# Kernel tuning notes

Measured on AMD Instinct MI355X. Metric: run time of the kernel, lower is better.

The kernel has to match this reference:

```python
import jax, jax.numpy as jnp
import numpy as np

V, D, H, C = 100000, 300, 16, 5
B, T = 256, 128


def setup_inputs() -> dict:
    key = jax.random.key(0)
    ks = jax.random.split(key, 8)
    s = 1.0 / np.sqrt(H).astype(np.float32)  # PyTorch LSTM/Linear init range
    x = jax.random.randint(ks[0], (B, T), 0, V)
    emb = jax.random.normal(ks[1], (V, D), jnp.float32) * 0.02
    W_ih = jax.random.uniform(ks[2], (4 * H, D), jnp.float32, -s, s)
    W_hh = jax.random.uniform(ks[3], (4 * H, H), jnp.float32, -s, s)
    b_ih = jax.random.uniform(ks[4], (4 * H,), jnp.float32, -s, s)
    b_hh = jax.random.uniform(ks[5], (4 * H,), jnp.float32, -s, s)
    W_out = jax.random.uniform(ks[6], (C, H), jnp.float32, -s, s)
    b_out = jax.random.uniform(ks[7], (C,), jnp.float32, -s, s)
    return dict(x=x, emb=emb, W_ih=W_ih, W_hh=W_hh, b_ih=b_ih, b_hh=b_hh,
                W_out=W_out, b_out=b_out)


def reference(x, emb, W_ih, W_hh, b_ih, b_hh, W_out, b_out):
    h_dim = W_hh.shape[1]
    xe = emb[x]  # [B,T,D] embedding lookup
    # Precompute input contribution to all 4 gates for all timesteps (one big GEMM).
    xg = jnp.einsum('btd,gd->btg', xe, W_ih) + b_ih + b_hh  # [B,T,4H]
    xg = jnp.transpose(xg, (1, 0, 2))  # [T,B,4H] time-major for scan
    b = x.shape[0]
    h0 = jnp.zeros((b, h_dim), xg.dtype)
    c0 = jnp.zeros((b, h_dim), xg.dtype)

    def step(carry, g_t):
        h, c = carry
        g = g_t + h @ W_hh.T  # [B,4H]
        i, f, gg, o = jnp.split(g, 4, axis=-1)  # PyTorch gate order: i,f,g,o
        i = jax.nn.sigmoid(i)
        f = jax.nn.sigmoid(f)
        gg = jnp.tanh(gg)
        o = jax.nn.sigmoid(o)
        c = f * c + i * gg
        h = o * jnp.tanh(c)
        return (h, c), h

    _, hs = jax.lax.scan(step, (h0, c0), xg)  # hs: [T,B,H]
    hs = jnp.transpose(hs, (1, 0, 2))  # [B,T,H]
    return hs @ W_out.T + b_out  # [B,T,C]
```

## Files before the change

### kernel.cpp

```cpp
#include <hip/hip_runtime.h>
#include <cstdint>

#define BB 256
#define TT 128
#define DD 300
#define HH 16
#define GG 64
#define CC 5
#define KC 60
#define NCH 5

__global__ __launch_bounds__(256) void lstm_fused_kernel(
    const int* __restrict__ x, const float* __restrict__ emb,
    const float* __restrict__ W_ih, const float* __restrict__ W_hh,
    const float* __restrict__ b_ih, const float* __restrict__ b_hh,
    const float* __restrict__ W_out, const float* __restrict__ b_out,
    float* __restrict__ out) {

  __shared__ float As[TT * KC];
  __shared__ float Ws[KC * 68];
  __shared__ float xgs[TT * GG];
  __shared__ float hsm[TT * HH];
  __shared__ int   xid[TT];

  const int t  = threadIdx.x;
  const int b  = blockIdx.x;
  const int tx = t & 15;
  const int ty = t >> 4;

  if (t < TT) xid[t] = x[b * TT + t];
  __syncthreads();

  const int na = (t < 128) ? 8 : 7;
  const int nw = (t < 192) ? 4 : 3;

  float4 apf[8];
  float4 wpf[4];

  auto load_chunk = [&](int dbase) {
#pragma unroll
    for (int i = 0; i < 8; i++) {
      if (i < na) {
        int u = t + 256 * i;
        int r = u / 15, f = u - r * 15;
        apf[i] = *(const float4*)(emb + (size_t)xid[r] * DD + dbase + 4 * f);
      }
    }
#pragma unroll
    for (int i = 0; i < 4; i++) {
      if (i < nw) {
        int u = t + 256 * i;
        int c = u / 15, f = u - c * 15;
        wpf[i] = *(const float4*)(W_ih + c * DD + dbase + 4 * f);
      }
    }
  };

  auto store_chunk = [&]() {
#pragma unroll
    for (int i = 0; i < 8; i++) {
      if (i < na) {
        int u = t + 256 * i;
        int r = u / 15, f = u - r * 15;
        *(float4*)&As[r * KC + 4 * f] = apf[i];
      }
    }
#pragma unroll
    for (int i = 0; i < 4; i++) {
      if (i < nw) {
        int u = t + 256 * i;
        int c = u / 15, f = u - c * 15;
        Ws[(4 * f + 0) * 68 + c] = wpf[i].x;
        Ws[(4 * f + 1) * 68 + c] = wpf[i].y;
        Ws[(4 * f + 2) * 68 + c] = wpf[i].z;
        Ws[(4 * f + 3) * 68 + c] = wpf[i].w;
      }
    }
  };

  float acc[8][4] = {};

  load_chunk(0);
  for (int ch = 0; ch < NCH; ch++) {
    if (ch > 0) __syncthreads();
    store_chunk();
    __syncthreads();
    if (ch + 1 < NCH) load_chunk((ch + 1) * KC);

#pragma unroll
    for (int q = 0; q < 15; q++) {
      float4 wc[4];
#pragma unroll
      for (int j = 0; j < 4; j++)
        wc[j] = *(const float4*)&Ws[(q * 4 + j) * 68 + tx * 4];
#pragma unroll
      for (int r = 0; r < 8; r++) {
        const int row = ty + 16 * r;
        float4 a = *(const float4*)&As[row * KC + q * 4];
#pragma unroll
        for (int c = 0; c < 4; c++) {
          acc[r][c] = fmaf(a.x, ((const float*)&wc[0])[c], acc[r][c]);
          acc[r][c] = fmaf(a.y, ((const float*)&wc[1])[c], acc[r][c]);
          acc[r][c] = fmaf(a.z, ((const float*)&wc[2])[c], acc[r][c]);
          acc[r][c] = fmaf(a.w, ((const float*)&wc[3])[c], acc[r][c]);
        }
      }
    }
  }

  float bias[4];
#pragma unroll
  for (int c = 0; c < 4; c++)
    bias[c] = b_ih[tx * 4 + c] + b_hh[tx * 4 + c];
#pragma unroll
  for (int r = 0; r < 8; r++) {
    const int row = ty + 16 * r;
    float4 o;
    o.x = acc[r][0] + bias[0];
    o.y = acc[r][1] + bias[1];
    o.z = acc[r][2] + bias[2];
    o.w = acc[r][3] + bias[3];
    *(float4*)&xgs[row * GG + tx * 4] = o;
  }
  __syncthreads();

  if (t < 64) {
    const int lane = t;
    const int k = lane & 15;
    const int gate = lane >> 4;
    const bool is_tanh = (gate == 2);
    const float L2E = 1.4426950408889634f;
    const float gscale = is_tanh ? (-2.0f * L2E) : (-L2E);

    float wh[16];
    {
      const float* wr = W_hh + lane * HH;
#pragma unroll
      for (int kk = 0; kk < 16; kk++) wh[kk] = wr[kk];
    }

    float c = 0.0f;
    float hu[16];
#pragma unroll
    for (int kk = 0; kk < 16; kk++) hu[kk] = 0.0f;

    float g = xgs[lane];
    for (int tstep = 0; tstep < TT; tstep++) {
      float gnext = xgs[((tstep + 1) & 127) * GG + lane];

      float a0 = fmaf(hu[0], wh[0], g);
      a0 = fmaf(hu[1], wh[1], a0);
      a0 = fmaf(hu[2], wh[2], a0);
      a0 = fmaf(hu[3], wh[3], a0);
      float a1 = hu[4] * wh[4];
      a1 = fmaf(hu[5], wh[5], a1);
      a1 = fmaf(hu[6], wh[6], a1);
      a1 = fmaf(hu[7], wh[7], a1);
      float a2 = hu[8] * wh[8];
      a2 = fmaf(hu[9], wh[9], a2);
      a2 = fmaf(hu[10], wh[10], a2);
      a2 = fmaf(hu[11], wh[11], a2);
      float a3 = hu[12] * wh[12];
      a3 = fmaf(hu[13], wh[13], a3);
      a3 = fmaf(hu[14], wh[14], a3);
      a3 = fmaf(hu[15], wh[15], a3);
      float gv_ = (a0 + a1) + (a2 + a3);

      float e = exp2f(gv_ * gscale);
      float s = __builtin_amdgcn_rcpf(1.0f + e);
      float act = is_tanh ? (2.0f * s - 1.0f) : s;

      float iv = __shfl(act, k);
      float fv = __shfl(act, k + 16);
      float gg = __shfl(act, k + 32);
      float ov = __shfl(act, k + 48);

      c = fmaf(fv, c, iv * gg);
      float e2 = exp2f(-2.0f * L2E * c);
      float tc = fmaf(2.0f, __builtin_amdgcn_rcpf(1.0f + e2), -1.0f);
      float hnew = ov * tc;

      if (lane < 16) hsm[tstep * HH + lane] = hnew;

#pragma unroll
      for (int kk = 0; kk < 16; kk++)
        hu[kk] = __uint_as_float(__builtin_amdgcn_readlane(__float_as_uint(hnew), kk));

      g = gnext;
    }
  }
  __syncthreads();

  float* outb = out + (size_t)b * TT * CC;
  for (int idx = t; idx < TT * CC; idx += 256) {
    int tt = idx / CC;
    int cc = idx - tt * CC;
    const float* wr = W_out + cc * HH;
    float accv = b_out[cc];
#pragma unroll
    for (int kk = 0; kk < 16; kk++) accv = fmaf(hsm[tt * HH + kk], wr[kk], accv);
    outb[idx] = accv;
  }
}

extern "C" void kernel_launch(void* const* d_in, const int* in_sizes, int n_in,
                              void* d_out, int out_size, void* d_ws, size_t ws_size,
                              hipStream_t stream) {
  const int*   x     = (const int*)d_in[0];
  const float* emb   = (const float*)d_in[1];
  const float* W_ih  = (const float*)d_in[2];
  const float* W_hh  = (const float*)d_in[3];
  const float* b_ih  = (const float*)d_in[4];
  const float* b_hh  = (const float*)d_in[5];
  const float* W_out = (const float*)d_in[6];
  const float* b_out = (const float*)d_in[7];
  float* out = (float*)d_out;

  lstm_fused_kernel<<<BB, 256, 0, stream>>>(x, emb, W_ih, W_hh, b_ih, b_hh,
                                            W_out, b_out, out);
}
```

Before: 236.5 us.

## Split fused LSTM into separate input-GEMM and recurrence kernels via workspace

Replaces the single fused kernel with two launches. The first is a GEMM over 64-row tiles (512 blocks) that gathers embeddings, multiplies by W_ih with an XOR-swizzled weight tile, and writes gate preactivations to a global workspace. The second is a one-wavefront-per-batch recurrence that streams xg chunks into shared memory while the scan runs, interleaves gate lanes so gate exchange uses DPP quad permutes instead of shuffles, and computes the output projection. This spreads the GEMM over more blocks and makes the serial recurrence a lighter kernel, at the cost of a global round trip for xg and a second launch.

```diff
diff --git a/kernel.cpp b/kernel.cpp
--- a/kernel.cpp
+++ b/kernel.cpp
@@ -8,38 +8,31 @@
 #define GG 64
 #define CC 5
 #define KC 60
-#define NCH 5
-
-__global__ __launch_bounds__(256) void lstm_fused_kernel(
+
+__global__ __launch_bounds__(256) void xg_gemm_kernel(
     const int* __restrict__ x, const float* __restrict__ emb,
-    const float* __restrict__ W_ih, const float* __restrict__ W_hh,
-    const float* __restrict__ b_ih, const float* __restrict__ b_hh,
-    const float* __restrict__ W_out, const float* __restrict__ b_out,
-    float* __restrict__ out) {
-
-  __shared__ float As[TT * KC];
-  __shared__ float Ws[KC * 68];
-  __shared__ float xgs[TT * GG];
-  __shared__ float hsm[TT * HH];
-  __shared__ int   xid[TT];
+    const float* __restrict__ W_ih, const float* __restrict__ b_ih,
+    const float* __restrict__ b_hh, float* __restrict__ xg) {
+
+  __shared__ float As[64 * KC];
+  __shared__ float Ws[KC * 64];
+  __shared__ int   xid[64];
 
   const int t  = threadIdx.x;
-  const int b  = blockIdx.x;
   const int tx = t & 15;
   const int ty = t >> 4;
-
-  if (t < TT) xid[t] = x[b * TT + t];
+  const int row0 = blockIdx.x * 64;
+
+  if (t < 64) xid[t] = x[row0 + t];
   __syncthreads();
 
-  const int na = (t < 128) ? 8 : 7;
-  const int nw = (t < 192) ? 4 : 3;
-
-  float4 apf[8];
-  float4 wpf[4];
+  const int na = (t < 192) ? 4 : 3;
+
+  float4 apf[4], wpf[4];
 
   auto load_chunk = [&](int dbase) {
 #pragma unroll
-    for (int i = 0; i < 8; i++) {
+    for (int i = 0; i < 4; i++) {
       if (i < na) {
         int u = t + 256 * i;
         int r = u / 15, f = u - r * 15;
@@ -48,7 +41,7 @@
     }
 #pragma unroll
     for (int i = 0; i < 4; i++) {
-      if (i < nw) {
+      if (i < na) {
         int u = t + 256 * i;
         int c = u / 15, f = u - c * 15;
         wpf[i] = *(const float4*)(W_ih + c * DD + dbase + 4 * f);
@@ -58,7 +51,7 @@
 
   auto store_chunk = [&]() {
 #pragma unroll
-    for (int i = 0; i < 8; i++) {
+    for (int i = 0; i < 4; i++) {
       if (i < na) {
         int u = t + 256 * i;
         int r = u / 15, f = u - r * 15;
@@ -67,42 +60,43 @@
     }
 #pragma unroll
     for (int i = 0; i < 4; i++) {
-      if (i < nw) {
+      if (i < na) {
         int u = t + 256 * i;
         int c = u / 15, f = u - c * 15;
-        Ws[(4 * f + 0) * 68 + c] = wpf[i].x;
-        Ws[(4 * f + 1) * 68 + c] = wpf[i].y;
-        Ws[(4 * f + 2) * 68 + c] = wpf[i].z;
-        Ws[(4 * f + 3) * 68 + c] = wpf[i].w;
+        int cp = (((c >> 2) ^ f) << 2) | (c & 3);
+        const float* w = (const float*)&wpf[i];
+        Ws[(4 * f + 0) * 64 + cp] = w[0];
+        Ws[(4 * f + 1) * 64 + cp] = w[1];
+        Ws[(4 * f + 2) * 64 + cp] = w[2];
+        Ws[(4 * f + 3) * 64 + cp] = w[3];
       }
     }
   };
 
-  float acc[8][4] = {};
+  float acc[4][4] = {};
 
   load_chunk(0);
-  for (int ch = 0; ch < NCH; ch++) {
+  for (int ch = 0; ch < 5; ch++) {
     if (ch > 0) __syncthreads();
     store_chunk();
     __syncthreads();
-    if (ch + 1 < NCH) load_chunk((ch + 1) * KC);
+    if (ch + 1 < 5) load_chunk((ch + 1) * KC);
 
 #pragma unroll
     for (int q = 0; q < 15; q++) {
       float4 wc[4];
 #pragma unroll
       for (int j = 0; j < 4; j++)
-        wc[j] = *(const float4*)&Ws[(q * 4 + j) * 68 + tx * 4];
-#pragma unroll
-      for (int r = 0; r < 8; r++) {
-        const int row = ty + 16 * r;
-        float4 a = *(const float4*)&As[row * KC + q * 4];
-#pragma unroll
-        for (int c = 0; c < 4; c++) {
-          acc[r][c] = fmaf(a.x, ((const float*)&wc[0])[c], acc[r][c]);
-          acc[r][c] = fmaf(a.y, ((const float*)&wc[1])[c], acc[r][c]);
-          acc[r][c] = fmaf(a.z, ((const float*)&wc[2])[c], acc[r][c]);
-          acc[r][c] = fmaf(a.w, ((const float*)&wc[3])[c], acc[r][c]);
+        wc[j] = *(const float4*)&Ws[(4 * q + j) * 64 + ((tx ^ q) << 2)];
+#pragma unroll
+      for (int r = 0; r < 4; r++) {
+        float4 a = *(const float4*)&As[(4 * ty + r) * KC + 4 * q];
+#pragma unroll
+        for (int m = 0; m < 4; m++) {
+          acc[r][m] = fmaf(a.x, ((const float*)&wc[0])[m], acc[r][m]);
+          acc[r][m] = fmaf(a.y, ((const float*)&wc[1])[m], acc[r][m]);
+          acc[r][m] = fmaf(a.z, ((const float*)&wc[2])[m], acc[r][m]);
+          acc[r][m] = fmaf(a.w, ((const float*)&wc[3])[m], acc[r][m]);
         }
       }
     }
@@ -110,45 +104,73 @@
 
   float bias[4];
 #pragma unroll
-  for (int c = 0; c < 4; c++)
-    bias[c] = b_ih[tx * 4 + c] + b_hh[tx * 4 + c];
-#pragma unroll
-  for (int r = 0; r < 8; r++) {
-    const int row = ty + 16 * r;
+  for (int m = 0; m < 4; m++)
+    bias[m] = b_ih[4 * tx + m] + b_hh[4 * tx + m];
+
+#pragma unroll
+  for (int r = 0; r < 4; r++) {
     float4 o;
     o.x = acc[r][0] + bias[0];
     o.y = acc[r][1] + bias[1];
     o.z = acc[r][2] + bias[2];
     o.w = acc[r][3] + bias[3];
-    *(float4*)&xgs[row * GG + tx * 4] = o;
-  }
-  __syncthreads();
-
-  if (t < 64) {
-    const int lane = t;
-    const int k = lane & 15;
-    const int gate = lane >> 4;
-    const bool is_tanh = (gate == 2);
-    const float L2E = 1.4426950408889634f;
-    const float gscale = is_tanh ? (-2.0f * L2E) : (-L2E);
-
-    float wh[16];
-    {
-      const float* wr = W_hh + lane * HH;
-#pragma unroll
-      for (int kk = 0; kk < 16; kk++) wh[kk] = wr[kk];
-    }
-
-    float c = 0.0f;
-    float hu[16];
-#pragma unroll
-    for (int kk = 0; kk < 16; kk++) hu[kk] = 0.0f;
-
-    float g = xgs[lane];
-    for (int tstep = 0; tstep < TT; tstep++) {
-      float gnext = xgs[((tstep + 1) & 127) * GG + lane];
-
-      float a0 = fmaf(hu[0], wh[0], g);
+    *(float4*)&xg[(size_t)(row0 + 4 * ty + r) * GG + 4 * tx] = o;
+  }
+}
+
+__global__ __launch_bounds__(64) void lstm_seq_kernel(
+    const float* __restrict__ xg, const float* __restrict__ W_hh,
+    const float* __restrict__ W_out, const float* __restrict__ b_out,
+    float* __restrict__ out) {
+
+  __shared__ float xgs[TT * GG];
+  __shared__ float hsm[TT * HH];
+
+  const int lane = threadIdx.x;
+  const int b = blockIdx.x;
+  const float4* __restrict__ src4 = (const float4*)(xg + (size_t)b * TT * GG);
+  float4* dst4 = (float4*)xgs;
+
+  const int k = lane >> 2;
+  const int g = lane & 3;
+  const int j = g * 16 + k;
+
+  float wh[16];
+  {
+    const float* wr = W_hh + j * HH;
+#pragma unroll
+    for (int kk = 0; kk < 16; kk++) wh[kk] = wr[kk];
+  }
+
+  float4 buf[8];
+#pragma unroll
+  for (int i = 0; i < 8; i++) buf[i] = src4[i * 64 + lane];
+#pragma unroll
+  for (int i = 0; i < 8; i++) dst4[i * 64 + lane] = buf[i];
+
+  const float L2E = 1.4426950408889634f;
+  const bool is_tanh = (g == 2);
+  const float gscale = is_tanh ? (-2.0f * L2E) : (-L2E);
+
+  float c = 0.0f;
+  float hu[16];
+#pragma unroll
+  for (int kk = 0; kk < 16; kk++) hu[kk] = 0.0f;
+
+  for (int ch = 0; ch < 4; ch++) {
+    if (ch < 3) {
+#pragma unroll
+      for (int i = 0; i < 8; i++)
+        buf[i] = src4[(ch + 1) * 512 + i * 64 + lane];
+    }
+
+    float gp = xgs[(ch * 32) * GG + j];
+#pragma unroll 4
+    for (int s = 0; s < 32; s++) {
+      const int ts = ch * 32 + s;
+      float gn = (s < 31) ? xgs[(ts + 1) * GG + j] : 0.0f;
+
+      float a0 = fmaf(hu[0], wh[0], gp);
       a0 = fmaf(hu[1], wh[1], a0);
       a0 = fmaf(hu[2], wh[2], a0);
       a0 = fmaf(hu[3], wh[3], a0);
@@ -164,41 +186,51 @@
       a3 = fmaf(hu[13], wh[13], a3);
       a3 = fmaf(hu[14], wh[14], a3);
       a3 = fmaf(hu[15], wh[15], a3);
-      float gv_ = (a0 + a1) + (a2 + a3);
-
-      float e = exp2f(gv_ * gscale);
-      float s = __builtin_amdgcn_rcpf(1.0f + e);
-      float act = is_tanh ? (2.0f * s - 1.0f) : s;
-
-      float iv = __shfl(act, k);
-      float fv = __shfl(act, k + 16);
-      float gg = __shfl(act, k + 32);
-      float ov = __shfl(act, k + 48);
+      float gv = (a0 + a1) + (a2 + a3);
+
+      float e = exp2f(gv * gscale);
+      float sg = __builtin_amdgcn_rcpf(1.0f + e);
+      float act = is_tanh ? fmaf(2.0f, sg, -1.0f) : sg;
+
+      int ai = __float_as_int(act);
+      float iv = __int_as_float(__builtin_amdgcn_update_dpp(ai, ai, 0x00, 0xF, 0xF, true));
+      float fv = __int_as_float(__builtin_amdgcn_update_dpp(ai, ai, 0x55, 0xF, 0xF, true));
+      float gg = __int_as_float(__builtin_amdgcn_update_dpp(ai, ai, 0xAA, 0xF, 0xF, true));
+      float ov = __int_as_float(__builtin_amdgcn_update_dpp(ai, ai, 0xFF, 0xF, 0xF, true));
 
       c = fmaf(fv, c, iv * gg);
       float e2 = exp2f(-2.0f * L2E * c);
       float tc = fmaf(2.0f, __builtin_amdgcn_rcpf(1.0f + e2), -1.0f);
       float hnew = ov * tc;
 
-      if (lane < 16) hsm[tstep * HH + lane] = hnew;
+      if (g == 0) hsm[ts * HH + k] = hnew;
 
 #pragma unroll
       for (int kk = 0; kk < 16; kk++)
-        hu[kk] = __uint_as_float(__builtin_amdgcn_readlane(__float_as_uint(hnew), kk));
-
-      g = gnext;
-    }
-  }
-  __syncthreads();
+        hu[kk] = __uint_as_float(
+            __builtin_amdgcn_readlane(__float_as_uint(hnew), 4 * kk));
+
+      gp = gn;
+    }
+
+    if (ch < 3) {
+#pragma unroll
+      for (int i = 0; i < 8; i++)
+        dst4[(ch + 1) * 512 + i * 64 + lane] = buf[i];
+    }
+  }
 
   float* outb = out + (size_t)b * TT * CC;
-  for (int idx = t; idx < TT * CC; idx += 256) {
+#pragma unroll
+  for (int ii = 0; ii < 10; ii++) {
+    int idx = ii * 64 + lane;
     int tt = idx / CC;
     int cc = idx - tt * CC;
     const float* wr = W_out + cc * HH;
     float accv = b_out[cc];
 #pragma unroll
-    for (int kk = 0; kk < 16; kk++) accv = fmaf(hsm[tt * HH + kk], wr[kk], accv);
+    for (int kk = 0; kk < 16; kk++)
+      accv = fmaf(hsm[tt * HH + kk], wr[kk], accv);
     outb[idx] = accv;
   }
 }
@@ -215,7 +247,8 @@
   const float* W_out = (const float*)d_in[6];
   const float* b_out = (const float*)d_in[7];
   float* out = (float*)d_out;
-
-  lstm_fused_kernel<<<BB, 256, 0, stream>>>(x, emb, W_ih, W_hh, b_ih, b_hh,
-                                            W_out, b_out, out);
+  float* xg  = (float*)d_ws;
+
+  xg_gemm_kernel<<<BB * TT / 64, 256, 0, stream>>>(x, emb, W_ih, b_ih, b_hh, xg);
+  lstm_seq_kernel<<<BB, 64, 0, stream>>>(xg, W_hh, W_out, b_out, out);
 }
```

Result: faster. 217.3 us (-8.1%).
